# Kernel tuning notes

Hardware: AMD Instinct MI355X
Metric: run time of the kernel (lower is better)

The kernel has to match this reference:

```python
import jax, jax.numpy as jnp
import numpy as np

EPS = 1e-5

def gn(x, w, b):
    # torch GroupNorm(num_groups=1, C) on [N, C]: normalize over channels per row
    m = jnp.mean(x, axis=-1, keepdims=True)
    v = jnp.mean((x - m) ** 2, axis=-1, keepdims=True)
    return (x - m) * jax.lax.rsqrt(v + EPS) * w + b

def att_layer(agts, ctr_d, hi, wi, nodes, p):
    (Wd1, bd1, Wd2, gnd2_w, gnd2_b, Wq, gnq_w, gnq_b,
     Wc1, gnc1_w, gnc1_b, Wc2, Wa, gnn_w, gnn_b, Wl, gnl_w, gnl_b) = p
    res = agts
    # dist MLP on edge ctr differences [E,2]
    d = jax.nn.relu(ctr_d @ Wd1.T + bd1)                     # [E, n_ctx]
    d = jax.nn.relu(gn(d @ Wd2.T, gnd2_w, gnd2_b))           # [E, n_ctx]
    # query from gathered actor features
    q = jax.nn.relu(gn(agts[hi] @ Wq.T, gnq_w, gnq_b))       # [E, n_ctx]
    # context: concat(dist, query, gathered lane feats) -> MLP
    cf = jnp.concatenate([d, q, nodes[wi]], axis=-1)         # [E, 3*n_ctx]
    cf = jax.nn.relu(gn(cf @ Wc1.T, gnc1_w, gnc1_b))         # [E, n_agt]
    cf = cf @ Wc2.T                                          # [E, n_agt]
    # scatter-aggregate onto actors
    a = agts @ Wa.T
    a = a.at[hi].add(cf)
    a = jax.nn.relu(gn(a, gnn_w, gnn_b))
    a = gn(a @ Wl.T, gnl_w, gnl_b)  # Linear with act=False
    return jax.nn.relu(a + res)

def setup_inputs() -> dict:
    key = jax.random.key(0)
    ks = jax.random.split(key, 20)
    M, N, E, D = 4000, 20000, 150000, 128
    s2 = 1.0 / np.sqrt(2.0)
    s128 = 1.0 / np.sqrt(128.0)
    s384 = 1.0 / np.sqrt(384.0)
    inp = {}
    inp["actors"] = jax.random.normal(ks[0], (M, D), jnp.float32)
    inp["nodes"] = jax.random.normal(ks[1], (N, D), jnp.float32)
    inp["actor_ctrs"] = jax.random.uniform(ks[2], (M, 2), jnp.float32)
    inp["node_ctrs"] = jax.random.uniform(ks[3], (N, 2), jnp.float32)
    inp["hi"] = jax.random.randint(ks[4], (E,), 0, M, dtype=jnp.int32)
    inp["wi"] = jax.random.randint(ks[5], (E,), 0, N, dtype=jnp.int32)
    inp["Wd1"] = jax.random.normal(ks[6], (2, D, 2), jnp.float32) * s2
    inp["bd1"] = jnp.zeros((2, D), jnp.float32)
    inp["Wd2"] = jax.random.normal(ks[7], (2, D, D), jnp.float32) * s128
    inp["gnd2_w"] = jnp.ones((2, D), jnp.float32)
    inp["gnd2_b"] = jnp.zeros((2, D), jnp.float32)
    inp["Wq"] = jax.random.normal(ks[8], (2, D, D), jnp.float32) * s128
    inp["gnq_w"] = jnp.ones((2, D), jnp.float32)
    inp["gnq_b"] = jnp.zeros((2, D), jnp.float32)
    inp["Wc1"] = jax.random.normal(ks[9], (2, D, 3 * D), jnp.float32) * s384
    inp["gnc1_w"] = jnp.ones((2, D), jnp.float32)
    inp["gnc1_b"] = jnp.zeros((2, D), jnp.float32)
    inp["Wc2"] = jax.random.normal(ks[10], (2, D, D), jnp.float32) * s128
    inp["Wa"] = jax.random.normal(ks[11], (2, D, D), jnp.float32) * s128
    inp["gnn_w"] = jnp.ones((2, D), jnp.float32)
    inp["gnn_b"] = jnp.zeros((2, D), jnp.float32)
    inp["Wl"] = jax.random.normal(ks[12], (2, D, D), jnp.float32) * s128
    inp["gnl_w"] = jnp.ones((2, D), jnp.float32)
    inp["gnl_b"] = jnp.zeros((2, D), jnp.float32)
    return inp

def reference(actors, nodes, actor_ctrs, node_ctrs, hi, wi,
              Wd1, bd1, Wd2, gnd2_w, gnd2_b, Wq, gnq_w, gnq_b,
              Wc1, gnc1_w, gnc1_b, Wc2, Wa, gnn_w, gnn_b, Wl, gnl_w, gnl_b):
    ctr_d = actor_ctrs[hi] - node_ctrs[wi]  # [E, 2], same edges for both layers
    stacked = (Wd1, bd1, Wd2, gnd2_w, gnd2_b, Wq, gnq_w, gnq_b,
               Wc1, gnc1_w, gnc1_b, Wc2, Wa, gnn_w, gnn_b, Wl, gnl_w, gnl_b)
    agts = actors
    for i in range(2):  # two Att layers
        p = tuple(t[i] for t in stacked)
        agts = att_layer(agts, ctr_d, hi, wi, nodes, p)
    return agts
```

## Files before the change

### kernel.cpp

```cpp
#include <hip/hip_runtime.h>

#define M_ACT 4000
#define NNODE 20000
#define NE 150000
#define DD 128
#define NT_E 586
#define NB_N2 313
#define HB 587
#define AB 63
#define ASTR 136
#define WSTR 72
#define BSTR 136

typedef __attribute__((ext_vector_type(8))) short bh8;
typedef __attribute__((ext_vector_type(4))) float vf4;

#define MFMA16(a, b, c) __builtin_amdgcn_mfma_f32_16x16x32_bf16((a), (b), (c), 0, 0, 0)
#define LGKM0() __asm__ volatile("s_waitcnt lgkmcnt(0)" ::: "memory")

__device__ __forceinline__ unsigned short f2bf(float f) {
    unsigned u = __float_as_uint(f);
    u = (u + 0x7fffu + ((u >> 16) & 1u)) >> 16;
    return (unsigned short)u;
}
__device__ __forceinline__ float bf2f(unsigned short s) {
    return __uint_as_float(((unsigned)s) << 16);
}

__device__ __forceinline__ void gn_stats8(const vf4* acc, float* mean, float* rs) {
    float s[4], q[4];
#pragma unroll
    for (int i = 0; i < 4; i++) {
        float a = 0.f, b = 0.f;
#pragma unroll
        for (int t = 0; t < 8; t++) { float v = acc[t][i]; a += v; b += v * v; }
        s[i] = a; q[i] = b;
    }
#pragma unroll
    for (int m = 1; m < 16; m <<= 1) {
#pragma unroll
        for (int i = 0; i < 4; i++) {
            s[i] += __shfl_xor(s[i], m, 64);
            q[i] += __shfl_xor(q[i], m, 64);
        }
    }
#pragma unroll
    for (int i = 0; i < 4; i++) {
        float mu = s[i] * (1.0f / 128.0f);
        float var = q[i] * (1.0f / 128.0f) - mu * mu;
        mean[i] = mu;
        rs[i] = rsqrtf(var + 1e-5f);
    }
}

template <bool RELU>
__device__ __forceinline__ void gn_to_lds(const vf4* acc, const float* __restrict__ gw,
                                          const float* __restrict__ gb, unsigned short* sm,
                                          int stride, int cb, int r0, int grp, int lm) {
    float mean[4], rs[4];
    gn_stats8(acc, mean, rs);
#pragma unroll
    for (int t = 0; t < 8; t++) {
        int c = 16 * t + lm;
        float w = gw[c], b = gb[c];
#pragma unroll
        for (int i = 0; i < 4; i++) {
            float y = (acc[t][i] - mean[i]) * rs[i] * w + b;
            if (RELU) y = fmaxf(y, 0.0f);
            sm[(r0 + grp * 4 + i) * stride + cb + c] = f2bf(y);
        }
    }
}

__device__ __forceinline__ void load_chunk(const unsigned short* __restrict__ src,
                                           unsigned short* dst, int tid) {
    for (int idx = tid; idx < 1152; idx += 256) {
        *(uint4*)&dst[idx * 8] = *(const uint4*)&src[idx * 8];
    }
}

__device__ __forceinline__ void q2_body(unsigned short* smA, unsigned short* smW,
                                        const unsigned short* __restrict__ wq,
                                        const unsigned short* __restrict__ wc,
                                        const float* __restrict__ gnq_w,
                                        const float* __restrict__ gnq_b,
                                        float* __restrict__ Q2, int m0, int tid) {
    const int wave = tid >> 6, lane = tid & 63, grp = lane >> 4, lm = lane & 15;
    const int r0 = wave * 16;
    const int arow = r0 + lm;
    vf4 acc[8];
#pragma unroll
    for (int t = 0; t < 8; t++) acc[t] = (vf4){0.f, 0.f, 0.f, 0.f};
    for (int ch = 0; ch < 2; ch++) {
        load_chunk(wq + ch * 9216, smW, tid);
        __syncthreads();
#pragma unroll
        for (int k0 = 0; k0 < 64; k0 += 32) {
            bh8 a = *(const bh8*)&smA[arow * ASTR + ch * 64 + k0 + grp * 8];
#pragma unroll
            for (int t = 0; t < 8; t++) {
                bh8 b = *(const bh8*)&smW[(16 * t + lm) * WSTR + k0 + grp * 8];
                acc[t] = MFMA16(a, b, acc[t]);
            }
        }
        __syncthreads();
    }
    gn_to_lds<true>(acc, gnq_w, gnq_b, smA, ASTR, 0, r0, grp, lm);

#pragma unroll
    for (int t = 0; t < 8; t++) acc[t] = (vf4){0.f, 0.f, 0.f, 0.f};
    for (int ch = 0; ch < 2; ch++) {
        load_chunk(wc + ch * 9216, smW, tid);
        __syncthreads();
#pragma unroll
        for (int k0 = 0; k0 < 64; k0 += 32) {
            bh8 a = *(const bh8*)&smA[arow * ASTR + ch * 64 + k0 + grp * 8];
#pragma unroll
            for (int t = 0; t < 8; t++) {
                bh8 b = *(const bh8*)&smW[(16 * t + lm) * WSTR + k0 + grp * 8];
                acc[t] = MFMA16(a, b, acc[t]);
            }
        }
        __syncthreads();
    }
#pragma unroll
    for (int t = 0; t < 8; t++) {
        int c = 16 * t + lm;
#pragma unroll
        for (int i = 0; i < 4; i++) {
            int m = m0 + r0 + grp * 4 + i;
            if (m < M_ACT) Q2[(size_t)m * DD + c] = acc[t][i];
        }
    }
}

__global__ void setup_kernel(const int* __restrict__ hi, int* __restrict__ hist,
                             const float* __restrict__ Wd2, const float* __restrict__ Wq,
                             const float* __restrict__ Wc1, const float* __restrict__ Wc2,
                             const float* __restrict__ Wa, const float* __restrict__ Wl,
                             unsigned short* __restrict__ wblob) {
    int b = blockIdx.x;
    if (b < HB) {
        int e = b * 256 + threadIdx.x;
        if (e < NE) atomicAdd(&hist[hi[e]], 1);
        return;
    }
    int ci = b - HB;
    int l = ci >> 4, r = ci & 15;
    const float* src;
    int kc, K;
    if (r < 2)       { src = Wd2 + l * 16384; kc = r;      K = 128; }
    else if (r < 4)  { src = Wq  + l * 16384; kc = r - 2;  K = 128; }
    else if (r < 10) { src = Wc1 + l * 49152; kc = r - 4;  K = 384; }
    else if (r < 12) { src = Wc2 + l * 16384; kc = r - 10; K = 128; }
    else if (r < 14) { src = Wa  + l * 16384; kc = r - 12; K = 128; }
    else             { src = Wl  + l * 16384; kc = r - 14; K = 128; }
    unsigned short* dst = wblob + (size_t)ci * 9216;
    for (int idx = threadIdx.x; idx < 9216; idx += 256) {
        int n = idx / 72, kk = idx - n * 72;
        float v = (kk < 64) ? src[n * K + kc * 64 + kk] : 0.f;
        dst[idx] = f2bf(v);
    }
}

__global__ void scan_kernel(const int* __restrict__ hist, int* __restrict__ cursor) {
    __shared__ int part[256];
    int t = threadIdx.x;
    int base = t * 16;
    int s = 0;
    if (base < M_ACT)
        for (int i = 0; i < 16; i++) s += hist[base + i];
    part[t] = s;
    __syncthreads();
    for (int d = 1; d < 256; d <<= 1) {
        int u = (t >= d) ? part[t - d] : 0;
        __syncthreads();
        part[t] += u;
        __syncthreads();
    }
    int excl = part[t] - s;
    if (base < M_ACT) {
        int run = excl;
        for (int i = 0; i < 16; i++) {
            cursor[base + i] = run;
            run += hist[base + i];
        }
    }
}

__global__ __launch_bounds__(256, 2) void mega0_kernel(
    const int* __restrict__ hi, const int* __restrict__ wi, int* __restrict__ cursor,
    int* __restrict__ hi_s, int* __restrict__ wi_s, const float* __restrict__ nodes,
    const unsigned short* __restrict__ wblob, float* __restrict__ N2_0,
    float* __restrict__ N2_1, const float* __restrict__ agts,
    const float* __restrict__ gnq_w, const float* __restrict__ gnq_b,
    float* __restrict__ Q2) {
    __shared__ unsigned short smA[64 * ASTR];
    __shared__ unsigned short smW[128 * WSTR];
    const int tid = threadIdx.x;
    int b = blockIdx.x;
    if (b < HB) {
        int e = b * 256 + tid;
        if (e < NE) {
            int h = hi[e];
            int p = atomicAdd(&cursor[h], 1);
            hi_s[p] = h;
            wi_s[p] = wi[e];
        }
        return;
    }
    b -= HB;
    const int wave = tid >> 6, lane = tid & 63, grp = lane >> 4, lm = lane & 15;
    const int r0 = wave * 16;
    const int arow = r0 + lm;
    if (b < 2 * NB_N2) {
        const int half = b / NB_N2;
        const int bx = b - half * NB_N2;
        const unsigned short* wblob_l = wblob + (size_t)half * 16 * 9216;
        float* __restrict__ N2 = half ? N2_1 : N2_0;
        const int n0 = bx * 64;
        for (int idx = tid; idx < 64 * 32; idx += 256) {
            int r = idx >> 5, q = idx & 31;
            int n = n0 + r;
            if (n >= NNODE) n = 0;
            const float4 v = *(const float4*)(nodes + (size_t)n * DD + q * 4);
            unsigned lo = (unsigned)f2bf(v.x) | ((unsigned)f2bf(v.y) << 16);
            unsigned hi2 = (unsigned)f2bf(v.z) | ((unsigned)f2bf(v.w) << 16);
            *(uint2*)&smA[r * ASTR + q * 4] = make_uint2(lo, hi2);
        }
        __syncthreads();
        vf4 acc[8];
#pragma unroll
        for (int t = 0; t < 8; t++) acc[t] = (vf4){0.f, 0.f, 0.f, 0.f};
        for (int ch = 0; ch < 2; ch++) {
            load_chunk(wblob_l + (8 + ch) * 9216, smW, tid);
            __syncthreads();
#pragma unroll
            for (int k0 = 0; k0 < 64; k0 += 32) {
                bh8 a = *(const bh8*)&smA[arow * ASTR + ch * 64 + k0 + grp * 8];
#pragma unroll
                for (int t = 0; t < 8; t++) {
                    bh8 bb = *(const bh8*)&smW[(16 * t + lm) * WSTR + k0 + grp * 8];
                    acc[t] = MFMA16(a, bb, acc[t]);
                }
            }
            __syncthreads();
        }
#pragma unroll
        for (int t = 0; t < 8; t++) {
            int c = 16 * t + lm;
#pragma unroll
            for (int i = 0; i < 4; i++) {
                int n = n0 + r0 + grp * 4 + i;
                if (n < NNODE) N2[(size_t)n * DD + c] = acc[t][i];
            }
        }
        return;
    }
    b -= 2 * NB_N2;
    const int m0 = b * 64;
    for (int idx = tid; idx < 64 * 32; idx += 256) {
        int r = idx >> 5, q = idx & 31;
        int m = m0 + r;
        if (m >= M_ACT) m = 0;
        const float4 v = *(const float4*)(agts + (size_t)m * DD + q * 4);
        unsigned lo = (unsigned)f2bf(v.x) | ((unsigned)f2bf(v.y) << 16);
        unsigned hi2 = (unsigned)f2bf(v.z) | ((unsigned)f2bf(v.w) << 16);
        *(uint2*)&smA[r * ASTR + q * 4] = make_uint2(lo, hi2);
    }
    __syncthreads();
    q2_body(smA, smW, wblob + 2 * 9216, wblob + 6 * 9216, gnq_w, gnq_b, Q2, m0, tid);
}

__global__ __launch_bounds__(512, 2) void edge_kernel(
    const float* __restrict__ actor_ctrs, const float* __restrict__ node_ctrs,
    const float* __restrict__ Wd1_l, const float* __restrict__ bd1_l,
    const float* __restrict__ Q2, const float* __restrict__ N2,
    const int* __restrict__ hi_s, const int* __restrict__ wi_s,
    const unsigned short* __restrict__ wblob_l,
    const float* __restrict__ gnd2_w, const float* __restrict__ gnd2_b,
    const float* __restrict__ gnc1_w, const float* __restrict__ gnc1_b,
    float* __restrict__ ssum, int* __restrict__ ctr) {
    __shared__ unsigned short smW[4 * 9216];
    __shared__ unsigned short smBuf[8][32 * BSTR];
    __shared__ float smWd1[3][128];
    __shared__ int smTile;
    {
        const int src0[4] = {0, 1, 4, 5};
#pragma unroll
        for (int s = 0; s < 4; s++)
            for (int idx = threadIdx.x; idx < 1152; idx += 512)
                *(uint4*)&smW[s * 9216 + idx * 8] =
                    *(const uint4*)&wblob_l[src0[s] * 9216 + idx * 8];
        for (int t = threadIdx.x; t < 128; t += 512) {
            smWd1[0][t] = Wd1_l[2 * t + 0];
            smWd1[1][t] = Wd1_l[2 * t + 1];
            smWd1[2][t] = bd1_l[t];
        }
    }
    const int wave = threadIdx.x >> 6, lane = threadIdx.x & 63;
    const int grp = lane >> 4, lm = lane & 15;
    unsigned short* buf = smBuf[wave];

    while (true) {
        __syncthreads();
        if (threadIdx.x == 0) smTile = atomicAdd(ctr, 1);
        __syncthreads();
        int tile = smTile;
        if (tile >= NT_E) break;
        int j0 = tile * 256 + wave * 32;
        if (j0 >= NE) continue;

        vf4 acc[2][8];
        int hg[2][4], wg[2][4];
        float cx[2], cy[2];
#pragma unroll
        for (int rt = 0; rt < 2; rt++) {
            int r = j0 + rt * 16 + lm;
            if (r > NE - 1) r = NE - 1;
            int hr = hi_s[r], wr = wi_s[r];
            cx[rt] = actor_ctrs[hr * 2 + 0] - node_ctrs[wr * 2 + 0];
            cy[rt] = actor_ctrs[hr * 2 + 1] - node_ctrs[wr * 2 + 1];
#pragma unroll
            for (int i = 0; i < 4; i++) {
                int j = j0 + rt * 16 + grp * 4 + i;
                if (j > NE - 1) j = NE - 1;
                hg[rt][i] = hi_s[j];
                wg[rt][i] = wi_s[j];
            }
        }
        bh8 a1[2][4];
#pragma unroll
        for (int ks = 0; ks < 4; ks++) {
            float wx[8], wy[8], wb[8];
#pragma unroll
            for (int e = 0; e < 8; e++) {
                int c = ks * 32 + grp * 8 + e;
                wx[e] = smWd1[0][c];
                wy[e] = smWd1[1][c];
                wb[e] = smWd1[2][c];
            }
#pragma unroll
            for (int rt = 0; rt < 2; rt++) {
                bh8 v;
#pragma unroll
                for (int e = 0; e < 8; e++) {
                    float x = fmaf(cy[rt], wy[e], fmaf(cx[rt], wx[e], wb[e]));
                    v[e] = (short)f2bf(fmaxf(x, 0.f));
                }
                a1[rt][ks] = v;
            }
        }
#pragma unroll
        for (int rt = 0; rt < 2; rt++)
#pragma unroll
            for (int t = 0; t < 8; t++) acc[rt][t] = (vf4){0.f, 0.f, 0.f, 0.f};
#pragma unroll
        for (int ks = 0; ks < 4; ks++) {
            bh8 B[8];
#pragma unroll
            for (int t = 0; t < 8; t++)
                B[t] = *(const bh8*)&smW[(ks >> 1) * 9216 + (16 * t + lm) * WSTR +
                                         (ks & 1) * 32 + grp * 8];
#pragma unroll
            for (int rt = 0; rt < 2; rt++)
#pragma unroll
                for (int t = 0; t < 8; t++) acc[rt][t] = MFMA16(a1[rt][ks], B[t], acc[rt][t]);
        }
        LGKM0();
#pragma unroll
        for (int rt = 0; rt < 2; rt++) {
            float mean[4], rs[4];
            gn_stats8(acc[rt], mean, rs);
#pragma unroll
            for (int t = 0; t < 8; t++) {
                int c = 16 * t + lm;
                float w = gnd2_w[c], b = gnd2_b[c];
#pragma unroll
                for (int i = 0; i < 4; i++) {
                    float y = (acc[rt][t][i] - mean[i]) * rs[i] * w + b;
                    buf[(rt * 16 + grp * 4 + i) * BSTR + c] = f2bf(fmaxf(y, 0.f));
                }
            }
        }
        LGKM0();
#pragma unroll
        for (int rt = 0; rt < 2; rt++)
#pragma unroll
            for (int t = 0; t < 8; t++) acc[rt][t] = (vf4){0.f, 0.f, 0.f, 0.f};
#pragma unroll
        for (int ks = 0; ks < 4; ks++) {
            bh8 B[8];
#pragma unroll
            for (int t = 0; t < 8; t++)
                B[t] = *(const bh8*)&smW[(2 + (ks >> 1)) * 9216 + (16 * t + lm) * WSTR +
                                         (ks & 1) * 32 + grp * 8];
#pragma unroll
            for (int rt = 0; rt < 2; rt++) {
                bh8 a = *(const bh8*)&buf[(rt * 16 + lm) * BSTR + ks * 32 + grp * 8];
#pragma unroll
                for (int t = 0; t < 8; t++) acc[rt][t] = MFMA16(a, B[t], acc[rt][t]);
            }
        }
#pragma unroll
        for (int rt = 0; rt < 2; rt++)
#pragma unroll
            for (int t = 0; t < 8; t++) {
                int c = 16 * t + lm;
#pragma unroll
                for (int i = 0; i < 4; i++)
                    acc[rt][t][i] +=
                        Q2[(size_t)hg[rt][i] * DD + c] + N2[(size_t)wg[rt][i] * DD + c];
            }
#pragma unroll
        for (int rt = 0; rt < 2; rt++) {
            float mean[4], rs[4];
            gn_stats8(acc[rt], mean, rs);
#pragma unroll
            for (int t = 0; t < 8; t++) {
                int c = 16 * t + lm;
                float w = gnc1_w[c], b = gnc1_b[c];
#pragma unroll
                for (int i = 0; i < 4; i++) {
                    float y = (acc[rt][t][i] - mean[i]) * rs[i] * w + b;
                    acc[rt][t][i] = fmaxf(y, 0.f);
                }
            }
        }
        {
            int hrem[2][4];
#pragma unroll
            for (int rt = 0; rt < 2; rt++)
#pragma unroll
                for (int i = 0; i < 4; i++) {
                    int j = j0 + rt * 16 + grp * 4 + i;
                    hrem[rt][i] = (j < NE) ? hg[rt][i] : -1;
                }
            while (true) {
                int hmin = 0x7fffffff;
#pragma unroll
                for (int rt = 0; rt < 2; rt++)
#pragma unroll
                    for (int i = 0; i < 4; i++)
                        if (hrem[rt][i] >= 0 && hrem[rt][i] < hmin) hmin = hrem[rt][i];
                hmin = min(hmin, __shfl_xor(hmin, 16, 64));
                hmin = min(hmin, __shfl_xor(hmin, 32, 64));
                if (hmin == 0x7fffffff) break;
                float p[8];
#pragma unroll
                for (int t = 0; t < 8; t++) p[t] = 0.f;
#pragma unroll
                for (int rt = 0; rt < 2; rt++)
#pragma unroll
                    for (int i = 0; i < 4; i++)
                        if (hrem[rt][i] == hmin) {
#pragma unroll
                            for (int t = 0; t < 8; t++) p[t] += acc[rt][t][i];
                            hrem[rt][i] = -1;
                        }
#pragma unroll
                for (int t = 0; t < 8; t++) {
                    p[t] += __shfl_xor(p[t], 16, 64);
                    p[t] += __shfl_xor(p[t], 32, 64);
                }
                if (grp == 0) {
#pragma unroll
                    for (int t = 0; t < 8; t++)
                        atomicAdd(&ssum[(size_t)hmin * DD + 16 * t + lm], p[t]);
                }
            }
        }
    }
}

__global__ __launch_bounds__(256, 2) void actor_q2_kernel(
    const float* __restrict__ agts, const float* __restrict__ ssum,
    const float* __restrict__ gnn_w, const float* __restrict__ gnn_b,
    const float* __restrict__ gnl_w, const float* __restrict__ gnl_b,
    const unsigned short* __restrict__ wblob, float* __restrict__ A1,
    const float* __restrict__ gnq_w1, const float* __restrict__ gnq_b1,
    float* __restrict__ Q2) {
    __shared__ unsigned short smA[64 * ASTR];
    __shared__ unsigned short smW[128 * WSTR];
    const int tid = threadIdx.x;
    const int wave = tid >> 6, lane = tid & 63, grp = lane >> 4, lm = lane & 15;
    const int m0 = blockIdx.x * 64;
    const int r0 = wave * 16;
    const int arow = r0 + lm;

    for (int idx = tid; idx < 64 * 32; idx += 256) {
        int r = idx >> 5, q = idx & 31;
        int m = m0 + r;
        if (m >= M_ACT) m = 0;
        const float4 v = *(const float4*)(ssum + (size_t)m * DD + q * 4);
        unsigned lo = (unsigned)f2bf(v.x) | ((unsigned)f2bf(v.y) << 16);
        unsigned hi2 = (unsigned)f2bf(v.z) | ((unsigned)f2bf(v.w) << 16);
        *(uint2*)&smA[r * ASTR + q * 4] = make_uint2(lo, hi2);
    }
    __syncthreads();

    vf4 acc[8];
#pragma unroll
    for (int t = 0; t < 8; t++) acc[t] = (vf4){0.f, 0.f, 0.f, 0.f};
    for (int ch = 0; ch < 2; ch++) {
        load_chunk(wblob + (10 + ch) * 9216, smW, tid);
        __syncthreads();
#pragma unroll
        for (int k0 = 0; k0 < 64; k0 += 32) {
            bh8 a = *(const bh8*)&smA[arow * ASTR + ch * 64 + k0 + grp * 8];
#pragma unroll
            for (int t = 0; t < 8; t++) {
                bh8 b = *(const bh8*)&smW[(16 * t + lm) * WSTR + k0 + grp * 8];
                acc[t] = MFMA16(a, b, acc[t]);
            }
        }
        __syncthreads();
    }
    for (int idx = tid; idx < 64 * 32; idx += 256) {
        int r = idx >> 5, q = idx & 31;
        int m = m0 + r;
        if (m >= M_ACT) m = 0;
        const float4 v = *(const float4*)(agts + (size_t)m * DD + q * 4);
        unsigned lo = (unsigned)f2bf(v.x) | ((unsigned)f2bf(v.y) << 16);
        unsigned hi2 = (unsigned)f2bf(v.z) | ((unsigned)f2bf(v.w) << 16);
        *(uint2*)&smA[r * ASTR + q * 4] = make_uint2(lo, hi2);
    }
    __syncthreads();
    for (int ch = 0; ch < 2; ch++) {
        load_chunk(wblob + (12 + ch) * 9216, smW, tid);
        __syncthreads();
#pragma unroll
        for (int k0 = 0; k0 < 64; k0 += 32) {
            bh8 a = *(const bh8*)&smA[arow * ASTR + ch * 64 + k0 + grp * 8];
#pragma unroll
            for (int t = 0; t < 8; t++) {
                bh8 b = *(const bh8*)&smW[(16 * t + lm) * WSTR + k0 + grp * 8];
                acc[t] = MFMA16(a, b, acc[t]);
            }
        }
        __syncthreads();
    }
    gn_to_lds<true>(acc, gnn_w, gnn_b, smA, ASTR, 0, r0, grp, lm);

#pragma unroll
    for (int t = 0; t < 8; t++) acc[t] = (vf4){0.f, 0.f, 0.f, 0.f};
    for (int ch = 0; ch < 2; ch++) {
        load_chunk(wblob + (14 + ch) * 9216, smW, tid);
        __syncthreads();
#pragma unroll
        for (int k0 = 0; k0 < 64; k0 += 32) {
            bh8 a = *(const bh8*)&smA[arow * ASTR + ch * 64 + k0 + grp * 8];
#pragma unroll
            for (int t = 0; t < 8; t++) {
                bh8 b = *(const bh8*)&smW[(16 * t + lm) * WSTR + k0 + grp * 8];
                acc[t] = MFMA16(a, b, acc[t]);
            }
        }
        __syncthreads();
    }
    {
        float mean[4], rs[4];
        gn_stats8(acc, mean, rs);
#pragma unroll
        for (int t = 0; t < 8; t++) {
            int c = 16 * t + lm;
            float w = gnl_w[c], b = gnl_b[c];
#pragma unroll
            for (int i = 0; i < 4; i++) {
                int m = m0 + r0 + grp * 4 + i;
                float y = (acc[t][i] - mean[i]) * rs[i] * w + b;
                float o = 0.f;
                if (m < M_ACT) {
                    o = fmaxf(y + agts[(size_t)m * DD + c], 0.f);
                    A1[(size_t)m * DD + c] = o;
                }
                smA[(r0 + grp * 4 + i) * ASTR + c] = f2bf(o);
            }
        }
    }
    q2_body(smA, smW, wblob + (16 + 2) * 9216, wblob + (16 + 6) * 9216, gnq_w1, gnq_b1, Q2,
            m0, tid);
}

__global__ __launch_bounds__(256, 2) void actor_kernel(
    const float* __restrict__ agts, const float* __restrict__ ssum,
    const float* __restrict__ gnn_w, const float* __restrict__ gnn_b,
    const float* __restrict__ gnl_w, const float* __restrict__ gnl_b,
    const unsigned short* __restrict__ wblob_l, float* __restrict__ dst) {
    __shared__ unsigned short smA[64 * ASTR];
    __shared__ unsigned short smW[128 * WSTR];
    const int tid = threadIdx.x;
    const int wave = tid >> 6, lane = tid & 63, grp = lane >> 4, lm = lane & 15;
    const int m0 = blockIdx.x * 64;
    const int r0 = wave * 16;
    const int arow = r0 + lm;

    for (int idx = tid; idx < 64 * 32; idx += 256) {
        int r = idx >> 5, q = idx & 31;
        int m = m0 + r;
        if (m >= M_ACT) m = 0;
        const float4 v = *(const float4*)(ssum + (size_t)m * DD + q * 4);
        unsigned lo = (unsigned)f2bf(v.x) | ((unsigned)f2bf(v.y) << 16);
        unsigned hi2 = (unsigned)f2bf(v.z) | ((unsigned)f2bf(v.w) << 16);
        *(uint2*)&smA[r * ASTR + q * 4] = make_uint2(lo, hi2);
    }
    __syncthreads();

    vf4 acc[8];
#pragma unroll
    for (int t = 0; t < 8; t++) acc[t] = (vf4){0.f, 0.f, 0.f, 0.f};
    for (int ch = 0; ch < 2; ch++) {
        load_chunk(wblob_l + (10 + ch) * 9216, smW, tid);
        __syncthreads();
#pragma unroll
        for (int k0 = 0; k0 < 64; k0 += 32) {
            bh8 a = *(const bh8*)&smA[arow * ASTR + ch * 64 + k0 + grp * 8];
#pragma unroll
            for (int t = 0; t < 8; t++) {
                bh8 b = *(const bh8*)&smW[(16 * t + lm) * WSTR + k0 + grp * 8];
                acc[t] = MFMA16(a, b, acc[t]);
            }
        }
        __syncthreads();
    }
    for (int idx = tid; idx < 64 * 32; idx += 256) {
        int r = idx >> 5, q = idx & 31;
        int m = m0 + r;
        if (m >= M_ACT) m = 0;
        const float4 v = *(const float4*)(agts + (size_t)m * DD + q * 4);
        unsigned lo = (unsigned)f2bf(v.x) | ((unsigned)f2bf(v.y) << 16);
        unsigned hi2 = (unsigned)f2bf(v.z) | ((unsigned)f2bf(v.w) << 16);
        *(uint2*)&smA[r * ASTR + q * 4] = make_uint2(lo, hi2);
    }
    __syncthreads();
    for (int ch = 0; ch < 2; ch++) {
        load_chunk(wblob_l + (12 + ch) * 9216, smW, tid);
        __syncthreads();
#pragma unroll
        for (int k0 = 0; k0 < 64; k0 += 32) {
            bh8 a = *(const bh8*)&smA[arow * ASTR + ch * 64 + k0 + grp * 8];
#pragma unroll
            for (int t = 0; t < 8; t++) {
                bh8 b = *(const bh8*)&smW[(16 * t + lm) * WSTR + k0 + grp * 8];
                acc[t] = MFMA16(a, b, acc[t]);
            }
        }
        __syncthreads();
    }
    gn_to_lds<true>(acc, gnn_w, gnn_b, smA, ASTR, 0, r0, grp, lm);

#pragma unroll
    for (int t = 0; t < 8; t++) acc[t] = (vf4){0.f, 0.f, 0.f, 0.f};
    for (int ch = 0; ch < 2; ch++) {
        load_chunk(wblob_l + (14 + ch) * 9216, smW, tid);
        __syncthreads();
#pragma unroll
        for (int k0 = 0; k0 < 64; k0 += 32) {
            bh8 a = *(const bh8*)&smA[arow * ASTR + ch * 64 + k0 + grp * 8];
#pragma unroll
            for (int t = 0; t < 8; t++) {
                bh8 b = *(const bh8*)&smW[(16 * t + lm) * WSTR + k0 + grp * 8];
                acc[t] = MFMA16(a, b, acc[t]);
            }
        }
        __syncthreads();
    }
    {
        float mean[4], rs[4];
        gn_stats8(acc, mean, rs);
#pragma unroll
        for (int t = 0; t < 8; t++) {
            int c = 16 * t + lm;
            float w = gnl_w[c], b = gnl_b[c];
#pragma unroll
            for (int i = 0; i < 4; i++) {
                int m = m0 + r0 + grp * 4 + i;
                if (m < M_ACT) {
                    float y = (acc[t][i] - mean[i]) * rs[i] * w + b;
                    y += agts[(size_t)m * DD + c];
                    dst[(size_t)m * DD + c] = fmaxf(y, 0.f);
                }
            }
        }
    }
}

extern "C" void kernel_launch(void* const* d_in, const int* in_sizes, int n_in,
                              void* d_out, int out_size, void* d_ws, size_t ws_size,
                              hipStream_t stream) {
    const float* actors = (const float*)d_in[0];
    const float* nodes = (const float*)d_in[1];
    const float* actor_ctrs = (const float*)d_in[2];
    const float* node_ctrs = (const float*)d_in[3];
    const int* hi = (const int*)d_in[4];
    const int* wi = (const int*)d_in[5];
    const float* Wd1 = (const float*)d_in[6];
    const float* bd1 = (const float*)d_in[7];
    const float* Wd2 = (const float*)d_in[8];
    const float* gnd2_w = (const float*)d_in[9];
    const float* gnd2_b = (const float*)d_in[10];
    const float* Wq = (const float*)d_in[11];
    const float* gnq_w = (const float*)d_in[12];
    const float* gnq_b = (const float*)d_in[13];
    const float* Wc1 = (const float*)d_in[14];
    const float* gnc1_w = (const float*)d_in[15];
    const float* gnc1_b = (const float*)d_in[16];
    const float* Wc2 = (const float*)d_in[17];
    const float* Wa = (const float*)d_in[18];
    const float* gnn_w = (const float*)d_in[19];
    const float* gnn_b = (const float*)d_in[20];
    const float* Wl = (const float*)d_in[21];
    const float* gnl_w = (const float*)d_in[22];
    const float* gnl_b = (const float*)d_in[23];
    float* out = (float*)d_out;

    char* ws = (char*)d_ws;
    unsigned short* wblob = (unsigned short*)ws;  ws += 2 * 16 * 9216 * 2;
    float* Q2 = (float*)ws;                       ws += (size_t)M_ACT * DD * 4;
    float* N2_0 = (float*)ws;                     ws += (size_t)NNODE * DD * 4;
    float* N2_1 = (float*)ws;                     ws += (size_t)NNODE * DD * 4;
    float* A1 = (float*)ws;                       ws += (size_t)M_ACT * DD * 4;
    int* cursor = (int*)ws;                       ws += M_ACT * 4;
    int* hi_s = (int*)ws;                         ws += NE * 4;
    int* wi_s = (int*)ws;                         ws += NE * 4;
    char* zbase = ws;
    int* hist = (int*)ws;                         ws += M_ACT * 4;
    int* ctr4 = (int*)ws;                         ws += 64;
    float* ssum0 = (float*)ws;                    ws += (size_t)M_ACT * DD * 4;
    float* ssum1 = (float*)ws;                    ws += (size_t)M_ACT * DD * 4;
    const size_t zbytes = (size_t)(ws - zbase);

    hipMemsetAsync(zbase, 0, zbytes, stream);
    setup_kernel<<<HB + 32, 256, 0, stream>>>(hi, hist, Wd2, Wq, Wc1, Wc2, Wa, Wl, wblob);
    scan_kernel<<<1, 256, 0, stream>>>(hist, cursor);

    const unsigned short* wb0 = wblob;
    const unsigned short* wb1 = wblob + 16 * 9216;

    mega0_kernel<<<HB + 2 * NB_N2 + AB, 256, 0, stream>>>(hi, wi, cursor, hi_s, wi_s, nodes,
                                                          wblob, N2_0, N2_1, actors, gnq_w,
                                                          gnq_b, Q2);
    edge_kernel<<<256, 512, 0, stream>>>(actor_ctrs, node_ctrs, Wd1, bd1, Q2, N2_0, hi_s,
                                         wi_s, wb0, gnd2_w, gnd2_b, gnc1_w, gnc1_b, ssum0,
                                         &ctr4[0]);
    actor_q2_kernel<<<AB, 256, 0, stream>>>(actors, ssum0, gnn_w, gnn_b, gnl_w, gnl_b, wblob,
                                            A1, gnq_w + 128, gnq_b + 128, Q2);
    edge_kernel<<<256, 512, 0, stream>>>(actor_ctrs, node_ctrs, Wd1 + 256, bd1 + 128, Q2,
                                         N2_1, hi_s, wi_s, wb1, gnd2_w + 128, gnd2_b + 128,
                                         gnc1_w + 128, gnc1_b + 128, ssum1, &ctr4[1]);
    actor_kernel<<<AB, 256, 0, stream>>>(A1, ssum1, gnn_w + 128, gnn_b + 128, gnl_w + 128,
                                         gnl_b + 128, wb1, out);
}
```

Baseline: 299.6 us.

## Split actor kernels into 16-row single-wave blocks and precompute agts@Wa early

The actor-stage kernels now run one wavefront per 16-row block (250 blocks instead of 63 four-wave blocks). They read weight B-fragments straight from global memory instead of staging them through LDS with block barriers. The layer-0 agts@Wa product moves into extra blocks of the first mega kernel, which overlap with the graph and node work, and the actor_q2 kernel adds the stored result. The aim is to shorten the serial tail kernels between the edge passes by raising parallelism and removing LDS weight staging. The costs are more global/L2 weight traffic per block and an extra [M,128] workspace buffer.

```diff
diff --git a/kernel.cpp b/kernel.cpp
--- a/kernel.cpp
+++ b/kernel.cpp
@@ -8,6 +8,7 @@
 #define NB_N2 313
 #define HB 587
 #define AB 63
+#define AB16 250
 #define ASTR 136
 #define WSTR 72
 #define BSTR 136
@@ -76,6 +77,32 @@
                                            unsigned short* dst, int tid) {
     for (int idx = tid; idx < 1152; idx += 256) {
         *(uint4*)&dst[idx * 8] = *(const uint4*)&src[idx * 8];
+    }
+}
+
+__device__ __forceinline__ void gemm16(const unsigned short* smA,
+                                       const unsigned short* __restrict__ w2ch, vf4* acc,
+                                       int grp, int lm) {
+#pragma unroll
+    for (int ks = 0; ks < 4; ks++) {
+        bh8 a = *(const bh8*)&smA[lm * ASTR + ks * 32 + grp * 8];
+#pragma unroll
+        for (int t = 0; t < 8; t++) {
+            bh8 b = *(const bh8*)&w2ch[(ks >> 1) * 9216 + (16 * t + lm) * WSTR +
+                                       (ks & 1) * 32 + grp * 8];
+            acc[t] = MFMA16(a, b, acc[t]);
+        }
+    }
+}
+
+__device__ __forceinline__ void stage16(const float* __restrict__ src, int m0,
+                                        unsigned short* smA, int lane) {
+    for (int idx = lane; idx < 16 * 32; idx += 64) {
+        int r = idx >> 5, q = idx & 31;
+        const float4 v = *(const float4*)(src + (size_t)(m0 + r) * DD + q * 4);
+        unsigned lo = (unsigned)f2bf(v.x) | ((unsigned)f2bf(v.y) << 16);
+        unsigned hi2 = (unsigned)f2bf(v.z) | ((unsigned)f2bf(v.w) << 16);
+        *(uint2*)&smA[r * ASTR + q * 4] = make_uint2(lo, hi2);
     }
 }
 
@@ -194,7 +221,7 @@
     const unsigned short* __restrict__ wblob, float* __restrict__ N2_0,
     float* __restrict__ N2_1, const float* __restrict__ agts,
     const float* __restrict__ gnq_w, const float* __restrict__ gnq_b,
-    float* __restrict__ Q2) {
+    float* __restrict__ Q2, float* __restrict__ Aa) {
     __shared__ unsigned short smA[64 * ASTR];
     __shared__ unsigned short smW[128 * WSTR];
     const int tid = threadIdx.x;
@@ -258,7 +285,7 @@
         return;
     }
     b -= 2 * NB_N2;
-    const int m0 = b * 64;
+    const int m0 = (b < AB ? b : b - AB) * 64;
     for (int idx = tid; idx < 64 * 32; idx += 256) {
         int r = idx >> 5, q = idx & 31;
         int m = m0 + r;
@@ -269,7 +296,36 @@
         *(uint2*)&smA[r * ASTR + q * 4] = make_uint2(lo, hi2);
     }
     __syncthreads();
-    q2_body(smA, smW, wblob + 2 * 9216, wblob + 6 * 9216, gnq_w, gnq_b, Q2, m0, tid);
+    if (b < AB) {
+        q2_body(smA, smW, wblob + 2 * 9216, wblob + 6 * 9216, gnq_w, gnq_b, Q2, m0, tid);
+        return;
+    }
+    vf4 acc[8];
+#pragma unroll
+    for (int t = 0; t < 8; t++) acc[t] = (vf4){0.f, 0.f, 0.f, 0.f};
+    for (int ch = 0; ch < 2; ch++) {
+        load_chunk(wblob + (12 + ch) * 9216, smW, tid);
+        __syncthreads();
+#pragma unroll
+        for (int k0 = 0; k0 < 64; k0 += 32) {
+            bh8 a = *(const bh8*)&smA[arow * ASTR + ch * 64 + k0 + grp * 8];
+#pragma unroll
+            for (int t = 0; t < 8; t++) {
+                bh8 bb = *(const bh8*)&smW[(16 * t + lm) * WSTR + k0 + grp * 8];
+                acc[t] = MFMA16(a, bb, acc[t]);
+            }
+        }
+        __syncthreads();
+    }
+#pragma unroll
+    for (int t = 0; t < 8; t++) {
+        int c = 16 * t + lm;
+#pragma unroll
+        for (int i = 0; i < 4; i++) {
+            int m = m0 + r0 + grp * 4 + i;
+            if (m < M_ACT) Aa[(size_t)m * DD + c] = acc[t][i];
+        }
+    }
 }
 
 __global__ __launch_bounds__(512, 2) void edge_kernel(
@@ -473,198 +529,98 @@
     }
 }
 
-__global__ __launch_bounds__(256, 2) void actor_q2_kernel(
+__global__ __launch_bounds__(64) void actor_q2_kernel(
     const float* __restrict__ agts, const float* __restrict__ ssum,
-    const float* __restrict__ gnn_w, const float* __restrict__ gnn_b,
-    const float* __restrict__ gnl_w, const float* __restrict__ gnl_b,
-    const unsigned short* __restrict__ wblob, float* __restrict__ A1,
-    const float* __restrict__ gnq_w1, const float* __restrict__ gnq_b1,
-    float* __restrict__ Q2) {
-    __shared__ unsigned short smA[64 * ASTR];
-    __shared__ unsigned short smW[128 * WSTR];
-    const int tid = threadIdx.x;
-    const int wave = tid >> 6, lane = tid & 63, grp = lane >> 4, lm = lane & 15;
-    const int m0 = blockIdx.x * 64;
-    const int r0 = wave * 16;
-    const int arow = r0 + lm;
-
-    for (int idx = tid; idx < 64 * 32; idx += 256) {
-        int r = idx >> 5, q = idx & 31;
-        int m = m0 + r;
-        if (m >= M_ACT) m = 0;
-        const float4 v = *(const float4*)(ssum + (size_t)m * DD + q * 4);
-        unsigned lo = (unsigned)f2bf(v.x) | ((unsigned)f2bf(v.y) << 16);
-        unsigned hi2 = (unsigned)f2bf(v.z) | ((unsigned)f2bf(v.w) << 16);
-        *(uint2*)&smA[r * ASTR + q * 4] = make_uint2(lo, hi2);
-    }
-    __syncthreads();
-
+    const float* __restrict__ Aa, const float* __restrict__ gnn_w,
+    const float* __restrict__ gnn_b, const float* __restrict__ gnl_w,
+    const float* __restrict__ gnl_b, const unsigned short* __restrict__ wblob,
+    float* __restrict__ A1, const float* __restrict__ gnq_w1,
+    const float* __restrict__ gnq_b1, float* __restrict__ Q2) {
+    __shared__ unsigned short smA[16 * ASTR];
+    const int lane = threadIdx.x, grp = lane >> 4, lm = lane & 15;
+    const int m0 = blockIdx.x * 16;
+
+    stage16(ssum, m0, smA, lane);
+    __syncthreads();
     vf4 acc[8];
 #pragma unroll
     for (int t = 0; t < 8; t++) acc[t] = (vf4){0.f, 0.f, 0.f, 0.f};
-    for (int ch = 0; ch < 2; ch++) {
-        load_chunk(wblob + (10 + ch) * 9216, smW, tid);
-        __syncthreads();
-#pragma unroll
-        for (int k0 = 0; k0 < 64; k0 += 32) {
-            bh8 a = *(const bh8*)&smA[arow * ASTR + ch * 64 + k0 + grp * 8];
-#pragma unroll
-            for (int t = 0; t < 8; t++) {
-                bh8 b = *(const bh8*)&smW[(16 * t + lm) * WSTR + k0 + grp * 8];
-                acc[t] = MFMA16(a, b, acc[t]);
-            }
-        }
-        __syncthreads();
-    }
-    for (int idx = tid; idx < 64 * 32; idx += 256) {
-        int r = idx >> 5, q = idx & 31;
-        int m = m0 + r;
-        if (m >= M_ACT) m = 0;
-        const float4 v = *(const float4*)(agts + (size_t)m * DD + q * 4);
-        unsigned lo = (unsigned)f2bf(v.x) | ((unsigned)f2bf(v.y) << 16);
-        unsigned hi2 = (unsigned)f2bf(v.z) | ((unsigned)f2bf(v.w) << 16);
-        *(uint2*)&smA[r * ASTR + q * 4] = make_uint2(lo, hi2);
-    }
-    __syncthreads();
-    for (int ch = 0; ch < 2; ch++) {
-        load_chunk(wblob + (12 + ch) * 9216, smW, tid);
-        __syncthreads();
-#pragma unroll
-        for (int k0 = 0; k0 < 64; k0 += 32) {
-            bh8 a = *(const bh8*)&smA[arow * ASTR + ch * 64 + k0 + grp * 8];
-#pragma unroll
-            for (int t = 0; t < 8; t++) {
-                bh8 b = *(const bh8*)&smW[(16 * t + lm) * WSTR + k0 + grp * 8];
-                acc[t] = MFMA16(a, b, acc[t]);
-            }
-        }
-        __syncthreads();
-    }
-    gn_to_lds<true>(acc, gnn_w, gnn_b, smA, ASTR, 0, r0, grp, lm);
-
-#pragma unroll
-    for (int t = 0; t < 8; t++) acc[t] = (vf4){0.f, 0.f, 0.f, 0.f};
-    for (int ch = 0; ch < 2; ch++) {
-        load_chunk(wblob + (14 + ch) * 9216, smW, tid);
-        __syncthreads();
-#pragma unroll
-        for (int k0 = 0; k0 < 64; k0 += 32) {
-            bh8 a = *(const bh8*)&smA[arow * ASTR + ch * 64 + k0 + grp * 8];
-#pragma unroll
-            for (int t = 0; t < 8; t++) {
-                bh8 b = *(const bh8*)&smW[(16 * t + lm) * WSTR + k0 + grp * 8];
-                acc[t] = MFMA16(a, b, acc[t]);
-            }
-        }
-        __syncthreads();
-    }
+    gemm16(smA, wblob + 10 * 9216, acc, grp, lm);
+#pragma unroll
+    for (int t = 0; t < 8; t++) {
+        int c = 16 * t + lm;
+#pragma unroll
+        for (int i = 0; i < 4; i++)
+            acc[t][i] += Aa[(size_t)(m0 + grp * 4 + i) * DD + c];
+    }
+    __syncthreads();
+    gn_to_lds<true>(acc, gnn_w, gnn_b, smA, ASTR, 0, 0, grp, lm);
+    __syncthreads();
+#pragma unroll
+    for (int t = 0; t < 8; t++) acc[t] = (vf4){0.f, 0.f, 0.f, 0.f};
+    gemm16(smA, wblob + 14 * 9216, acc, grp, lm);
     {
         float mean[4], rs[4];
         gn_stats8(acc, mean, rs);
+        __syncthreads();
 #pragma unroll
         for (int t = 0; t < 8; t++) {
             int c = 16 * t + lm;
             float w = gnl_w[c], b = gnl_b[c];
 #pragma unroll
             for (int i = 0; i < 4; i++) {
-                int m = m0 + r0 + grp * 4 + i;
-                float y = (acc[t][i] - mean[i]) * rs[i] * w + b;
-                float o = 0.f;
-                if (m < M_ACT) {
-                    o = fmaxf(y + agts[(size_t)m * DD + c], 0.f);
-                    A1[(size_t)m * DD + c] = o;
-                }
-                smA[(r0 + grp * 4 + i) * ASTR + c] = f2bf(o);
-            }
-        }
-    }
-    q2_body(smA, smW, wblob + (16 + 2) * 9216, wblob + (16 + 6) * 9216, gnq_w1, gnq_b1, Q2,
-            m0, tid);
-}
-
-__global__ __launch_bounds__(256, 2) void actor_kernel(
-    const float* __restrict__ agts, const float* __restrict__ ssum,
+                int m = m0 + grp * 4 + i;
+                float y = (acc[t][i] - mean[i]) * rs[i] * w + b + agts[(size_t)m * DD + c];
+                float o = fmaxf(y, 0.f);
+                A1[(size_t)m * DD + c] = o;
+                smA[(grp * 4 + i) * ASTR + c] = f2bf(o);
+            }
+        }
+    }
+    __syncthreads();
+#pragma unroll
+    for (int t = 0; t < 8; t++) acc[t] = (vf4){0.f, 0.f, 0.f, 0.f};
+    gemm16(smA, wblob + (16 + 2) * 9216, acc, grp, lm);
+    __syncthreads();
+    gn_to_lds<true>(acc, gnq_w1, gnq_b1, smA, ASTR, 0, 0, grp, lm);
+    __syncthreads();
+#pragma unroll
+    for (int t = 0; t < 8; t++) acc[t] = (vf4){0.f, 0.f, 0.f, 0.f};
+    gemm16(smA, wblob + (16 + 6) * 9216, acc, grp, lm);
+#pragma unroll
+    for (int t = 0; t < 8; t++) {
+        int c = 16 * t + lm;
+#pragma unroll
+        for (int i = 0; i < 4; i++)
+            Q2[(size_t)(m0 + grp * 4 + i) * DD + c] = acc[t][i];
+    }
+}
+
+__global__ __launch_bounds__(64) void actor_kernel(
+    const float* __restrict__ A1, const float* __restrict__ ssum,
     const float* __restrict__ gnn_w, const float* __restrict__ gnn_b,
     const float* __restrict__ gnl_w, const float* __restrict__ gnl_b,
     const unsigned short* __restrict__ wblob_l, float* __restrict__ dst) {
-    __shared__ unsigned short smA[64 * ASTR];
-    __shared__ unsigned short smW[128 * WSTR];
-    const int tid = threadIdx.x;
-    const int wave = tid >> 6, lane = tid & 63, grp = lane >> 4, lm = lane & 15;
-    const int m0 = blockIdx.x * 64;
-    const int r0 = wave * 16;
-    const int arow = r0 + lm;
-
-    for (int idx = tid; idx < 64 * 32; idx += 256) {
-        int r = idx >> 5, q = idx & 31;
-        int m = m0 + r;
-        if (m >= M_ACT) m = 0;
-        const float4 v = *(const float4*)(ssum + (size_t)m * DD + q * 4);
-        unsigned lo = (unsigned)f2bf(v.x) | ((unsigned)f2bf(v.y) << 16);
-        unsigned hi2 = (unsigned)f2bf(v.z) | ((unsigned)f2bf(v.w) << 16);
-        *(uint2*)&smA[r * ASTR + q * 4] = make_uint2(lo, hi2);
-    }
-    __syncthreads();
-
+    __shared__ unsigned short smA[16 * ASTR];
+    const int lane = threadIdx.x, grp = lane >> 4, lm = lane & 15;
+    const int m0 = blockIdx.x * 16;
+
+    stage16(ssum, m0, smA, lane);
+    __syncthreads();
     vf4 acc[8];
 #pragma unroll
     for (int t = 0; t < 8; t++) acc[t] = (vf4){0.f, 0.f, 0.f, 0.f};
-    for (int ch = 0; ch < 2; ch++) {
-        load_chunk(wblob_l + (10 + ch) * 9216, smW, tid);
-        __syncthreads();
-#pragma unroll
-        for (int k0 = 0; k0 < 64; k0 += 32) {
-            bh8 a = *(const bh8*)&smA[arow * ASTR + ch * 64 + k0 + grp * 8];
-#pragma unroll
-            for (int t = 0; t < 8; t++) {
-                bh8 b = *(const bh8*)&smW[(16 * t + lm) * WSTR + k0 + grp * 8];
-                acc[t] = MFMA16(a, b, acc[t]);
-            }
-        }
-        __syncthreads();
-    }
-    for (int idx = tid; idx < 64 * 32; idx += 256) {
-        int r = idx >> 5, q = idx & 31;
-        int m = m0 + r;
-        if (m >= M_ACT) m = 0;
-        const float4 v = *(const float4*)(agts + (size_t)m * DD + q * 4);
-        unsigned lo = (unsigned)f2bf(v.x) | ((unsigned)f2bf(v.y) << 16);
-        unsigned hi2 = (unsigned)f2bf(v.z) | ((unsigned)f2bf(v.w) << 16);
-        *(uint2*)&smA[r * ASTR + q * 4] = make_uint2(lo, hi2);
-    }
-    __syncthreads();
-    for (int ch = 0; ch < 2; ch++) {
-        load_chunk(wblob_l + (12 + ch) * 9216, smW, tid);
-        __syncthreads();
-#pragma unroll
-        for (int k0 = 0; k0 < 64; k0 += 32) {
-            bh8 a = *(const bh8*)&smA[arow * ASTR + ch * 64 + k0 + grp * 8];
-#pragma unroll
-            for (int t = 0; t < 8; t++) {
-                bh8 b = *(const bh8*)&smW[(16 * t + lm) * WSTR + k0 + grp * 8];
-                acc[t] = MFMA16(a, b, acc[t]);
-            }
-        }
-        __syncthreads();
-    }
-    gn_to_lds<true>(acc, gnn_w, gnn_b, smA, ASTR, 0, r0, grp, lm);
-
-#pragma unroll
-    for (int t = 0; t < 8; t++) acc[t] = (vf4){0.f, 0.f, 0.f, 0.f};
-    for (int ch = 0; ch < 2; ch++) {
-        load_chunk(wblob_l + (14 + ch) * 9216, smW, tid);
-        __syncthreads();
-#pragma unroll
-        for (int k0 = 0; k0 < 64; k0 += 32) {
-            bh8 a = *(const bh8*)&smA[arow * ASTR + ch * 64 + k0 + grp * 8];
-#pragma unroll
-            for (int t = 0; t < 8; t++) {
-                bh8 b = *(const bh8*)&smW[(16 * t + lm) * WSTR + k0 + grp * 8];
-                acc[t] = MFMA16(a, b, acc[t]);
-            }
-        }
-        __syncthreads();
-    }
+    gemm16(smA, wblob_l + 10 * 9216, acc, grp, lm);
+    __syncthreads();
+    stage16(A1, m0, smA, lane);
+    __syncthreads();
+    gemm16(smA, wblob_l + 12 * 9216, acc, grp, lm);
+    __syncthreads();
+    gn_to_lds<true>(acc, gnn_w, gnn_b, smA, ASTR, 0, 0, grp, lm);
+    __syncthreads();
+#pragma unroll
+    for (int t = 0; t < 8; t++) acc[t] = (vf4){0.f, 0.f, 0.f, 0.f};
+    gemm16(smA, wblob_l + 14 * 9216, acc, grp, lm);
     {
         float mean[4], rs[4];
         gn_stats8(acc, mean, rs);
@@ -674,12 +630,9 @@
             float w = gnl_w[c], b = gnl_b[c];
 #pragma unroll
             for (int i = 0; i < 4; i++) {
-                int m = m0 + r0 + grp * 4 + i;
-                if (m < M_ACT) {
-                    float y = (acc[t][i] - mean[i]) * rs[i] * w + b;
-                    y += agts[(size_t)m * DD + c];
-                    dst[(size_t)m * DD + c] = fmaxf(y, 0.f);
-                }
+                int m = m0 + grp * 4 + i;
+                float y = (acc[t][i] - mean[i]) * rs[i] * w + b + A1[(size_t)m * DD + c];
+                dst[(size_t)m * DD + c] = fmaxf(y, 0.f);
             }
         }
     }
@@ -720,6 +673,7 @@
     float* N2_0 = (float*)ws;                     ws += (size_t)NNODE * DD * 4;
     float* N2_1 = (float*)ws;                     ws += (size_t)NNODE * DD * 4;
     float* A1 = (float*)ws;                       ws += (size_t)M_ACT * DD * 4;
+    float* Aa = (float*)ws;                       ws += (size_t)M_ACT * DD * 4;
     int* cursor = (int*)ws;                       ws += M_ACT * 4;
     int* hi_s = (int*)ws;                         ws += NE * 4;
     int* wi_s = (int*)ws;                         ws += NE * 4;
@@ -737,17 +691,17 @@
     const unsigned short* wb0 = wblob;
     const unsigned short* wb1 = wblob + 16 * 9216;
 
-    mega0_kernel<<<HB + 2 * NB_N2 + AB, 256, 0, stream>>>(hi, wi, cursor, hi_s, wi_s, nodes,
-                                                          wblob, N2_0, N2_1, actors, gnq_w,
-                                                          gnq_b, Q2);
+    mega0_kernel<<<HB + 2 * NB_N2 + 2 * AB, 256, 0, stream>>>(hi, wi, cursor, hi_s, wi_s,
+                                                              nodes, wblob, N2_0, N2_1,
+                                                              actors, gnq_w, gnq_b, Q2, Aa);
     edge_kernel<<<256, 512, 0, stream>>>(actor_ctrs, node_ctrs, Wd1, bd1, Q2, N2_0, hi_s,
                                          wi_s, wb0, gnd2_w, gnd2_b, gnc1_w, gnc1_b, ssum0,
                                          &ctr4[0]);
-    actor_q2_kernel<<<AB, 256, 0, stream>>>(actors, ssum0, gnn_w, gnn_b, gnl_w, gnl_b, wblob,
-                                            A1, gnq_w + 128, gnq_b + 128, Q2);
+    actor_q2_kernel<<<AB16, 64, 0, stream>>>(actors, ssum0, Aa, gnn_w, gnn_b, gnl_w, gnl_b,
+                                             wblob, A1, gnq_w + 128, gnq_b + 128, Q2);
     edge_kernel<<<256, 512, 0, stream>>>(actor_ctrs, node_ctrs, Wd1 + 256, bd1 + 128, Q2,
                                          N2_1, hi_s, wi_s, wb1, gnd2_w + 128, gnd2_b + 128,
                                          gnc1_w + 128, gnc1_b + 128, ssum1, &ctr4[1]);
-    actor_kernel<<<AB, 256, 0, stream>>>(A1, ssum1, gnn_w + 128, gnn_b + 128, gnl_w + 128,
-                                         gnl_b + 128, wb1, out);
-}
+    actor_kernel<<<AB16, 64, 0, stream>>>(A1, ssum1, gnn_w + 128, gnn_b + 128, gnl_w + 128,
+                                          gnl_b + 128, wb1, out);
+}
```

New measurement: 278.5 us. -7.0%, faster.
